# Performance work log

Measured on AMD Instinct MI355X. Metric: run time of the kernel, lower is better.

Reference implementation:

```python
import jax, jax.numpy as jnp
import numpy as np

N_EMBED = 1024
HEAD_SIZE = 128
B, T = 8, 2048

def setup_inputs() -> dict:
    key = jax.random.key(0)
    kx, kq, kk, kv = jax.random.split(key, 4)
    x = jax.random.normal(kx, (B, T, N_EMBED), dtype=jnp.float32)
    s = N_EMBED ** -0.5
    Wq = jax.random.normal(kq, (N_EMBED, HEAD_SIZE), dtype=jnp.float32) * s
    Wk = jax.random.normal(kk, (N_EMBED, HEAD_SIZE), dtype=jnp.float32) * s
    Wv = jax.random.normal(kv, (N_EMBED, HEAD_SIZE), dtype=jnp.float32) * s
    return {"x": x, "Wq": Wq, "Wk": Wk, "Wv": Wv}

def reference(x, Wq, Wk, Wv):
    # x: [B, T, C]; single causal attention head, eval mode (dropout = identity).
    Bb, Tt, C = x.shape
    q = x @ Wq  # [B, T, H]
    k = x @ Wk  # [B, T, H]
    v = x @ Wv  # [B, T, H]
    # NOTE: original scales by C**-0.5 with C = n_embed (input dim), not head_size.
    wgt = jnp.einsum('bqh,bkh->bqk', q, k) * (C ** -0.5)  # [B, T, T]
    causal = jnp.tril(jnp.ones((Tt, Tt), dtype=bool))
    wgt = jnp.where(causal, wgt, -jnp.inf)
    wgt = jax.nn.softmax(wgt, axis=-1)
    return wgt @ v  # [B, T, H]
```

## Files before the change

### kernel.cpp

```cpp
#include <hip/hip_runtime.h>
#include <hip/hip_bf16.h>

#define B_  8
#define T_  2048
#define C_  1024
#define H_  128

using f32x4  = __attribute__((ext_vector_type(4))) float;
using bf16x8 = __attribute__((ext_vector_type(8))) short;

__device__ __forceinline__ unsigned short f2bf(float f) {
    union { float f; unsigned u; } v; v.f = f;
    unsigned r = v.u + 0x7FFFu + ((v.u >> 16) & 1u);
    return (unsigned short)(r >> 16);
}

template<int C>
__device__ __forceinline__ float dppf(float v) {
    return __int_as_float(__builtin_amdgcn_update_dpp(0, __float_as_int(v), C, 0xF, 0xF, true));
}
#define DPPRED_MAX(v) { v = fmaxf(v, dppf<0xB1>(v)); v = fmaxf(v, dppf<0x4E>(v)); \
                        v = fmaxf(v, dppf<0x141>(v)); v = fmaxf(v, dppf<0x140>(v)); }
#define DPPRED_SUM(v) { v = v + dppf<0xB1>(v); v = v + dppf<0x4E>(v); \
                        v = v + dppf<0x141>(v); v = v + dppf<0x140>(v); }

__global__ void wconv_kernel(const float* __restrict__ Wq,
                             const float* __restrict__ Wk,
                             const float* __restrict__ Wv,
                             unsigned short* __restrict__ Wt) {
    int id  = blockIdx.x * 256 + threadIdx.x;
    int col = id % 384;
    int k   = id / 384;
    const float* W = (col < 128) ? Wq : ((col < 256) ? Wk : Wv);
    float v = W[k * H_ + (col & 127)];
    if (col < 128) v *= 0.03125f;
    Wt[(size_t)col * C_ + k] = f2bf(v);
}

__launch_bounds__(512, 2)
__global__ void gemm_kernel(const float* __restrict__ x,
                            const unsigned short* __restrict__ Wt,
                            unsigned short* __restrict__ qb,
                            unsigned short* __restrict__ kb,
                            unsigned short* __restrict__ vT) {
    __shared__ unsigned short As[2][64][40];

    const int tid  = threadIdx.x;
    const int wave = tid >> 6;
    const int lane = tid & 63;
    const int lo = lane & 15, hi = lane >> 4;
    const int row0 = blockIdx.x * 64;
    const int col0 = wave * 48;
    const int srow = tid >> 3;
    const int sk4  = (tid & 7) * 4;

    const float* xbase = x + (size_t)(row0 + srow) * C_ + sk4;

    f32x4 acc[4][3];
    #pragma unroll
    for (int rt = 0; rt < 4; ++rt)
        #pragma unroll
        for (int ct = 0; ct < 3; ++ct)
            acc[rt][ct] = f32x4{0.f, 0.f, 0.f, 0.f};

    float4 f0 = *(const float4*)(xbase);
    float4 f1 = *(const float4*)(xbase + 32);
    float4 f2 = *(const float4*)(xbase + 64);
    bf16x8 bc[3], bn[3];
    #pragma unroll
    for (int ct = 0; ct < 3; ++ct) {
        const unsigned short* wp = Wt + (size_t)(col0 + ct * 16 + lo) * C_ + 8 * hi;
        bc[ct] = *(const bf16x8*)(wp);
        bn[ct] = *(const bf16x8*)(wp + 32);
    }
    {
        unsigned a0 = f2bf(f0.x) | ((unsigned)f2bf(f0.y) << 16);
        unsigned a1 = f2bf(f0.z) | ((unsigned)f2bf(f0.w) << 16);
        *(uint2*)&As[0][srow][sk4] = uint2{a0, a1};
    }
    __syncthreads();

    for (int k = 0; k < 32; ++k) {
        const int cur = k & 1;

        float4 fn = f2;
        if (k < 29) fn = *(const float4*)(xbase + (k + 3) * 32);
        bf16x8 b2[3];
        const bool ldb2 = (k < 30);
        if (ldb2) {
            #pragma unroll
            for (int ct = 0; ct < 3; ++ct)
                b2[ct] = *(const bf16x8*)(Wt + (size_t)(col0 + ct * 16 + lo) * C_ + (k + 2) * 32 + 8 * hi);
        }

        bf16x8 af[4];
        #pragma unroll
        for (int rt = 0; rt < 4; ++rt)
            af[rt] = *(const bf16x8*)(&As[cur][rt * 16 + lo][8 * hi]);
        #pragma unroll
        for (int rt = 0; rt < 4; ++rt)
            #pragma unroll
            for (int ct = 0; ct < 3; ++ct)
                acc[rt][ct] = __builtin_amdgcn_mfma_f32_16x16x32_bf16(af[rt], bc[ct], acc[rt][ct], 0, 0, 0);

        if (k < 31) {
            unsigned a0 = f2bf(f1.x) | ((unsigned)f2bf(f1.y) << 16);
            unsigned a1 = f2bf(f1.z) | ((unsigned)f2bf(f1.w) << 16);
            *(uint2*)&As[cur ^ 1][srow][sk4] = uint2{a0, a1};
        }
        __syncthreads();

        f1 = f2; f2 = fn;
        bc[0] = bn[0]; bc[1] = bn[1]; bc[2] = bn[2];
        if (ldb2) { bn[0] = b2[0]; bn[1] = b2[1]; bn[2] = b2[2]; }
    }

    #pragma unroll
    for (int ct = 0; ct < 3; ++ct) {
        int col = col0 + ct * 16 + lo;
        int head = col >> 7;
        int h = col & 127;
        #pragma unroll
        for (int rt = 0; rt < 4; ++rt) {
            #pragma unroll
            for (int r = 0; r < 4; ++r) {
                int rg = row0 + rt * 16 + 4 * hi + r;
                unsigned short val = f2bf(acc[rt][ct][r]);
                if (head == 0)      qb[(size_t)rg * H_ + h] = val;
                else if (head == 1) kb[(size_t)rg * H_ + h] = val;
                else {
                    int b = rg >> 11, t = rg & (T_ - 1);
                    vT[((size_t)b * H_ + h) * T_ + t] = val;
                }
            }
        }
    }
}

__launch_bounds__(512, 2)
__global__ void attn1_kernel(const unsigned short* __restrict__ qb,
                             const unsigned short* __restrict__ kb,
                             const unsigned short* __restrict__ vT,
                             float* __restrict__ Opart,
                             float* __restrict__ MLpart) {
    __shared__ unsigned short Ks[64 * 128];
    __shared__ unsigned short Vs[128 * 64];
    __shared__ unsigned short Ps[8][16][72];

    const int tid  = threadIdx.x;
    const int wave = tid >> 6;
    const int lane = tid & 63;
    const int lo = lane & 15, hi = lane >> 4;

    const int bid   = blockIdx.x;
    const int b     = bid & 7;
    const int chunk = (bid >> 3) & 7;
    const int qt    = 7 - (bid >> 6);
    if (chunk > qt) return;

    const int kv_begin = chunk << 8;
    const size_t bT = (size_t)b * T_;
    const int qrow0 = (qt << 8) + wave * 32;

    const int krow = tid >> 3, kcol = (tid & 7) * 2;
    const int vrow = tid >> 2, vcol = (tid & 3) * 2;
    const unsigned short* kgsrc = kb + (bT + krow) * H_ + kcol * 8;
    const unsigned short* vgsrc = vT + ((size_t)b * H_ + vrow) * T_ + vcol * 8;
    unsigned short* kdst0 = &Ks[krow * 128 + ((kcol ^ (krow & 7)) * 8)];
    unsigned short* kdst1 = &Ks[krow * 128 + (((kcol + 1) ^ (krow & 7)) * 8)];
    unsigned short* vdst0 = &Vs[vrow * 64 + ((vcol ^ (vrow & 7)) * 8)];
    unsigned short* vdst1 = &Vs[vrow * 64 + (((vcol + 1) ^ (vrow & 7)) * 8)];

    bf16x8 qf[2][4];
    #pragma unroll
    for (int q2 = 0; q2 < 2; ++q2)
        #pragma unroll
        for (int kc = 0; kc < 4; ++kc)
            qf[q2][kc] = *(const bf16x8*)(qb + (bT + qrow0 + 16 * q2 + lo) * H_ + kc * 32 + 8 * hi);

    float m[2][4], l[2][4];
    f32x4 o[2][8];
    #pragma unroll
    for (int q2 = 0; q2 < 2; ++q2)
        #pragma unroll
        for (int r = 0; r < 4; ++r) { m[q2][r] = -1e30f; l[q2][r] = 0.f; }
    #pragma unroll
    for (int q2 = 0; q2 < 2; ++q2)
        #pragma unroll
        for (int ct = 0; ct < 8; ++ct) o[q2][ct] = f32x4{0.f, 0.f, 0.f, 0.f};

    uint4 kr0 = *(const uint4*)(kgsrc + (size_t)kv_begin * H_);
    uint4 kr1 = *(const uint4*)(kgsrc + (size_t)kv_begin * H_ + 8);
    uint4 vr0 = *(const uint4*)(vgsrc + kv_begin);
    uint4 vr1 = *(const uint4*)(vgsrc + kv_begin + 8);

    for (int t = 0; t < 4; ++t) {
        const int kv0 = kv_begin + t * 64;
        __syncthreads();
        *(uint4*)kdst0 = kr0;
        *(uint4*)kdst1 = kr1;
        *(uint4*)vdst0 = vr0;
        *(uint4*)vdst1 = vr1;
        __syncthreads();
        if (t < 3) {
            const int kvn = kv0 + 64;
            kr0 = *(const uint4*)(kgsrc + (size_t)kvn * H_);
            kr1 = *(const uint4*)(kgsrc + (size_t)kvn * H_ + 8);
            vr0 = *(const uint4*)(vgsrc + kvn);
            vr1 = *(const uint4*)(vgsrc + kvn + 8);
        }
        if (kv0 > qrow0 + 31) continue;

        f32x4 s[2][4];
        #pragma unroll
        for (int q2 = 0; q2 < 2; ++q2)
            #pragma unroll
            for (int ct4 = 0; ct4 < 4; ++ct4) s[q2][ct4] = f32x4{0.f, 0.f, 0.f, 0.f};
        __builtin_amdgcn_s_setprio(1);
        #pragma unroll
        for (int ct4 = 0; ct4 < 4; ++ct4) {
            const int row = ct4 * 16 + lo;
            #pragma unroll
            for (int kc = 0; kc < 4; ++kc) {
                bf16x8 kf = *(const bf16x8*)&Ks[row * 128 + (((kc * 4 + hi) ^ (row & 7)) * 8)];
                s[0][ct4] = __builtin_amdgcn_mfma_f32_16x16x32_bf16(qf[0][kc], kf, s[0][ct4], 0, 0, 0);
                s[1][ct4] = __builtin_amdgcn_mfma_f32_16x16x32_bf16(qf[1][kc], kf, s[1][ct4], 0, 0, 0);
            }
        }
        __builtin_amdgcn_s_setprio(0);

        if (kv0 + 63 >= qrow0) {
            #pragma unroll
            for (int q2 = 0; q2 < 2; ++q2)
                #pragma unroll
                for (int ct4 = 0; ct4 < 4; ++ct4)
                    #pragma unroll
                    for (int r = 0; r < 4; ++r)
                        if (kv0 + ct4 * 16 + lo > qrow0 + 16 * q2 + 4 * hi + r)
                            s[q2][ct4][r] = -1e30f;
        }

        float alpha[2][4];
        #pragma unroll
        for (int q2 = 0; q2 < 2; ++q2) {
            #pragma unroll
            for (int r = 0; r < 4; ++r) {
                float pm = fmaxf(fmaxf(s[q2][0][r], s[q2][1][r]), fmaxf(s[q2][2][r], s[q2][3][r]));
                DPPRED_MAX(pm);
                float mn = fmaxf(m[q2][r], pm);
                alpha[q2][r] = __expf(m[q2][r] - mn);
                m[q2][r] = mn;
                #pragma unroll
                for (int ct4 = 0; ct4 < 4; ++ct4) s[q2][ct4][r] = __expf(s[q2][ct4][r] - mn);
                float rs = (s[q2][0][r] + s[q2][1][r]) + (s[q2][2][r] + s[q2][3][r]);
                DPPRED_SUM(rs);
                l[q2][r] = l[q2][r] * alpha[q2][r] + rs;
            }
        }
        #pragma unroll
        for (int q2 = 0; q2 < 2; ++q2)
            #pragma unroll
            for (int ct = 0; ct < 8; ++ct)
                #pragma unroll
                for (int r = 0; r < 4; ++r) o[q2][ct][r] *= alpha[q2][r];

        bf16x8 pa[2][2];
        #pragma unroll
        for (int q2 = 0; q2 < 2; ++q2) {
            #pragma unroll
            for (int ct4 = 0; ct4 < 4; ++ct4)
                #pragma unroll
                for (int r = 0; r < 4; ++r)
                    Ps[wave][4 * hi + r][ct4 * 16 + lo] = f2bf(s[q2][ct4][r]);
            pa[q2][0] = *(const bf16x8*)&Ps[wave][lo][8 * hi];
            pa[q2][1] = *(const bf16x8*)&Ps[wave][lo][32 + 8 * hi];
        }

        __builtin_amdgcn_s_setprio(1);
        #pragma unroll
        for (int ct = 0; ct < 8; ++ct) {
            const int row = ct * 16 + lo;
            #pragma unroll
            for (int half = 0; half < 2; ++half) {
                bf16x8 vf = *(const bf16x8*)&Vs[row * 64 + (((half * 4 + hi) ^ (row & 7)) * 8)];
                o[0][ct] = __builtin_amdgcn_mfma_f32_16x16x32_bf16(pa[0][half], vf, o[0][ct], 0, 0, 0);
                o[1][ct] = __builtin_amdgcn_mfma_f32_16x16x32_bf16(pa[1][half], vf, o[1][ct], 0, 0, 0);
            }
        }
        __builtin_amdgcn_s_setprio(0);
    }

    const int slot = b * 36 + ((qt * (qt + 1)) >> 1) + chunk;
    float* op = Opart + (size_t)slot * 32768 + (size_t)(wave * 32) * 128;
    #pragma unroll
    for (int q2 = 0; q2 < 2; ++q2)
        #pragma unroll
        for (int ct = 0; ct < 8; ++ct)
            #pragma unroll
            for (int r = 0; r < 4; ++r)
                op[(16 * q2 + 4 * hi + r) * 128 + ct * 16 + lo] = o[q2][ct][r];
    if (lo == 0) {
        #pragma unroll
        for (int q2 = 0; q2 < 2; ++q2)
            #pragma unroll
            for (int r = 0; r < 4; ++r) {
                int base = slot * 512 + (wave * 32 + 16 * q2 + 4 * hi + r) * 2;
                MLpart[base]     = m[q2][r];
                MLpart[base + 1] = l[q2][r];
            }
    }
}

__launch_bounds__(128)
__global__ void attn2_kernel(const float* __restrict__ Opart,
                             const float* __restrict__ MLpart,
                             float* __restrict__ out) {
    const int bid = blockIdx.x;
    const int b   = bid & 7;
    const int qt  = (bid >> 3) & 7;
    const int sub = bid >> 6;
    const int nch = qt + 1;
    const int slot0 = b * 36 + ((qt * (qt + 1)) >> 1);

    const int tid  = threadIdx.x;
    const int row  = tid >> 2;
    const int h0   = (tid & 3) * 32;
    const int srow = sub * 32 + row;

    float M = -1e30f;
    for (int c = 0; c < nch; ++c)
        M = fmaxf(M, MLpart[(slot0 + c) * 512 + srow * 2]);
    float L = 0.f;
    for (int c = 0; c < nch; ++c) {
        float mc = MLpart[(slot0 + c) * 512 + srow * 2];
        float lc = MLpart[(slot0 + c) * 512 + srow * 2 + 1];
        L += lc * __expf(mc - M);
    }

    float4 acc[8];
    #pragma unroll
    for (int j = 0; j < 8; ++j) acc[j] = float4{0.f, 0.f, 0.f, 0.f};
    for (int c = 0; c < nch; ++c) {
        float wc = __expf(MLpart[(slot0 + c) * 512 + srow * 2] - M);
        const float4* src = (const float4*)(Opart + (size_t)(slot0 + c) * 32768 + (size_t)srow * 128 + h0);
        #pragma unroll
        for (int j = 0; j < 8; ++j) {
            float4 v = src[j];
            acc[j].x += wc * v.x; acc[j].y += wc * v.y;
            acc[j].z += wc * v.z; acc[j].w += wc * v.w;
        }
    }
    float inv = 1.f / L;
    float4* dst = (float4*)(out + ((size_t)b * T_ + qt * 256 + srow) * H_ + h0);
    #pragma unroll
    for (int j = 0; j < 8; ++j) {
        float4 v = acc[j];
        dst[j] = float4{v.x * inv, v.y * inv, v.z * inv, v.w * inv};
    }
}

extern "C" void kernel_launch(void* const* d_in, const int* in_sizes, int n_in,
                              void* d_out, int out_size, void* d_ws, size_t ws_size,
                              hipStream_t stream) {
    const float* x  = (const float*)d_in[0];
    const float* Wq = (const float*)d_in[1];
    const float* Wk = (const float*)d_in[2];
    const float* Wv = (const float*)d_in[3];
    float* out = (float*)d_out;

    char* ws = (char*)d_ws;
    unsigned short* Wt  = (unsigned short*)ws;
    unsigned short* qbf = (unsigned short*)(ws + (size_t)384 * 1024 * 2);
    unsigned short* kbf = qbf + (size_t)B_ * T_ * H_;
    unsigned short* vTf = kbf + (size_t)B_ * T_ * H_;
    float* Opart  = (float*)(vTf + (size_t)B_ * T_ * H_);
    float* MLpart = (float*)((char*)Opart + (size_t)288 * 32768 * 4);

    wconv_kernel<<<(384 * 1024) / 256, 256, 0, stream>>>(Wq, Wk, Wv, Wt);
    gemm_kernel<<<B_ * T_ / 64, 512, 0, stream>>>(x, Wt, qbf, kbf, vTf);
    attn1_kernel<<<512, 512, 0, stream>>>(qbf, kbf, vTf, Opart, MLpart);
    attn2_kernel<<<512, 128, 0, stream>>>(Opart, MLpart, out);
}
```

Before: 89.29 us.

## Retile QKV projection GEMM to 32-row blocks with 64-wide K steps

The QKV projection GEMM moves from 64-row blocks with 8 waves of 48 columns to 32-row blocks with 4 waves of 96 columns each, launching twice as many blocks. Each K step now covers 64 elements, which halves the loop trips and the number of barriers. The explicit multi-stage register prefetch of x and W fragments is dropped in favour of loading W fragments directly each iteration. This adds more blocks and fewer syncs, but re-reads W from global/L2 more often per output row and exposes W load latency without software pipelining.

```diff
diff --git a/kernel.cpp b/kernel.cpp
--- a/kernel.cpp
+++ b/kernel.cpp
@@ -37,91 +37,92 @@
     Wt[(size_t)col * C_ + k] = f2bf(v);
 }
 
-__launch_bounds__(512, 2)
+__launch_bounds__(256, 2)
 __global__ void gemm_kernel(const float* __restrict__ x,
                             const unsigned short* __restrict__ Wt,
                             unsigned short* __restrict__ qb,
                             unsigned short* __restrict__ kb,
                             unsigned short* __restrict__ vT) {
-    __shared__ unsigned short As[2][64][40];
+    __shared__ unsigned short As[2][32][72];
 
     const int tid  = threadIdx.x;
     const int wave = tid >> 6;
     const int lane = tid & 63;
     const int lo = lane & 15, hi = lane >> 4;
-    const int row0 = blockIdx.x * 64;
-    const int col0 = wave * 48;
+    const int row0 = blockIdx.x * 32;
+    const int col0 = wave * 96;
     const int srow = tid >> 3;
-    const int sk4  = (tid & 7) * 4;
-
-    const float* xbase = x + (size_t)(row0 + srow) * C_ + sk4;
-
-    f32x4 acc[4][3];
-    #pragma unroll
-    for (int rt = 0; rt < 4; ++rt)
-        #pragma unroll
-        for (int ct = 0; ct < 3; ++ct)
+    const int sk   = (tid & 7) * 8;
+
+    const float* xbase = x + (size_t)(row0 + srow) * C_ + sk;
+
+    f32x4 acc[2][6];
+    #pragma unroll
+    for (int rt = 0; rt < 2; ++rt)
+        #pragma unroll
+        for (int ct = 0; ct < 6; ++ct)
             acc[rt][ct] = f32x4{0.f, 0.f, 0.f, 0.f};
 
-    float4 f0 = *(const float4*)(xbase);
-    float4 f1 = *(const float4*)(xbase + 32);
-    float4 f2 = *(const float4*)(xbase + 64);
-    bf16x8 bc[3], bn[3];
-    #pragma unroll
-    for (int ct = 0; ct < 3; ++ct) {
-        const unsigned short* wp = Wt + (size_t)(col0 + ct * 16 + lo) * C_ + 8 * hi;
-        bc[ct] = *(const bf16x8*)(wp);
-        bn[ct] = *(const bf16x8*)(wp + 32);
-    }
     {
+        float4 f0 = *(const float4*)(xbase);
+        float4 f1 = *(const float4*)(xbase + 4);
         unsigned a0 = f2bf(f0.x) | ((unsigned)f2bf(f0.y) << 16);
         unsigned a1 = f2bf(f0.z) | ((unsigned)f2bf(f0.w) << 16);
-        *(uint2*)&As[0][srow][sk4] = uint2{a0, a1};
+        unsigned a2 = f2bf(f1.x) | ((unsigned)f2bf(f1.y) << 16);
+        unsigned a3 = f2bf(f1.z) | ((unsigned)f2bf(f1.w) << 16);
+        *(uint4*)&As[0][srow][sk] = uint4{a0, a1, a2, a3};
     }
     __syncthreads();
 
-    for (int k = 0; k < 32; ++k) {
+    for (int k = 0; k < 16; ++k) {
         const int cur = k & 1;
 
-        float4 fn = f2;
-        if (k < 29) fn = *(const float4*)(xbase + (k + 3) * 32);
-        bf16x8 b2[3];
-        const bool ldb2 = (k < 30);
-        if (ldb2) {
-            #pragma unroll
-            for (int ct = 0; ct < 3; ++ct)
-                b2[ct] = *(const bf16x8*)(Wt + (size_t)(col0 + ct * 16 + lo) * C_ + (k + 2) * 32 + 8 * hi);
-        }
-
-        bf16x8 af[4];
-        #pragma unroll
-        for (int rt = 0; rt < 4; ++rt)
-            af[rt] = *(const bf16x8*)(&As[cur][rt * 16 + lo][8 * hi]);
-        #pragma unroll
-        for (int rt = 0; rt < 4; ++rt)
-            #pragma unroll
-            for (int ct = 0; ct < 3; ++ct)
-                acc[rt][ct] = __builtin_amdgcn_mfma_f32_16x16x32_bf16(af[rt], bc[ct], acc[rt][ct], 0, 0, 0);
-
-        if (k < 31) {
-            unsigned a0 = f2bf(f1.x) | ((unsigned)f2bf(f1.y) << 16);
-            unsigned a1 = f2bf(f1.z) | ((unsigned)f2bf(f1.w) << 16);
-            *(uint2*)&As[cur ^ 1][srow][sk4] = uint2{a0, a1};
+        float4 f0, f1;
+        if (k < 15) {
+            f0 = *(const float4*)(xbase + (k + 1) * 64);
+            f1 = *(const float4*)(xbase + (k + 1) * 64 + 4);
+        }
+
+        bf16x8 bf[6][2];
+        #pragma unroll
+        for (int ct = 0; ct < 6; ++ct) {
+            const unsigned short* wp = Wt + (size_t)(col0 + ct * 16 + lo) * C_ + k * 64 + 8 * hi;
+            bf[ct][0] = *(const bf16x8*)(wp);
+            bf[ct][1] = *(const bf16x8*)(wp + 32);
+        }
+
+        bf16x8 af[2][2];
+        #pragma unroll
+        for (int rt = 0; rt < 2; ++rt)
+            #pragma unroll
+            for (int kc = 0; kc < 2; ++kc)
+                af[rt][kc] = *(const bf16x8*)(&As[cur][rt * 16 + lo][kc * 32 + 8 * hi]);
+
+        #pragma unroll
+        for (int kc = 0; kc < 2; ++kc)
+            #pragma unroll
+            for (int ct = 0; ct < 6; ++ct)
+                #pragma unroll
+                for (int rt = 0; rt < 2; ++rt)
+                    acc[rt][ct] = __builtin_amdgcn_mfma_f32_16x16x32_bf16(af[rt][kc], bf[ct][kc], acc[rt][ct], 0, 0, 0);
+
+        if (k < 15) {
+            unsigned a0 = f2bf(f0.x) | ((unsigned)f2bf(f0.y) << 16);
+            unsigned a1 = f2bf(f0.z) | ((unsigned)f2bf(f0.w) << 16);
+            unsigned a2 = f2bf(f1.x) | ((unsigned)f2bf(f1.y) << 16);
+            unsigned a3 = f2bf(f1.z) | ((unsigned)f2bf(f1.w) << 16);
+            *(uint4*)&As[cur ^ 1][srow][sk] = uint4{a0, a1, a2, a3};
         }
         __syncthreads();
-
-        f1 = f2; f2 = fn;
-        bc[0] = bn[0]; bc[1] = bn[1]; bc[2] = bn[2];
-        if (ldb2) { bn[0] = b2[0]; bn[1] = b2[1]; bn[2] = b2[2]; }
-    }
-
-    #pragma unroll
-    for (int ct = 0; ct < 3; ++ct) {
+    }
+
+    #pragma unroll
+    for (int ct = 0; ct < 6; ++ct) {
         int col = col0 + ct * 16 + lo;
         int head = col >> 7;
         int h = col & 127;
         #pragma unroll
-        for (int rt = 0; rt < 4; ++rt) {
+        for (int rt = 0; rt < 2; ++rt) {
             #pragma unroll
             for (int r = 0; r < 4; ++r) {
                 int rg = row0 + rt * 16 + 4 * hi + r;
@@ -377,7 +378,7 @@
     float* MLpart = (float*)((char*)Opart + (size_t)288 * 32768 * 4);
 
     wconv_kernel<<<(384 * 1024) / 256, 256, 0, stream>>>(Wq, Wk, Wv, Wt);
-    gemm_kernel<<<B_ * T_ / 64, 512, 0, stream>>>(x, Wt, qbf, kbf, vTf);
+    gemm_kernel<<<B_ * T_ / 32, 256, 0, stream>>>(x, Wt, qbf, kbf, vTf);
     attn1_kernel<<<512, 512, 0, stream>>>(qbf, kbf, vTf, Opart, MLpart);
     attn2_kernel<<<512, 128, 0, stream>>>(Opart, MLpart, out);
 }
```

Result: slower. 114.5 us (+28.2%).

## Stage weight tiles into LDS via direct global-to-LDS loads and split GEMM columns

Applied to the files above, without the earlier changes.

The weight conversion now writes Wt in a k-tiled, MFMA-fragment-friendly layout, so the GEMM can copy each 32-wide k slice straight into shared memory with global_load_lds instead of having every wave load B fragments from global memory into registers. The projection GEMM is split into two column halves per 64-row block, using 256-thread blocks and twice as many blocks, and the x tile load is widened to 8 floats per thread. The MFMA section is wrapped in s_setprio. This aims to cut redundant global weight traffic and register pressure and to improve occupancy, at the cost of reading and converting each x row twice across the two column-half blocks.

```diff
diff --git a/kernel.cpp b/kernel.cpp
--- a/kernel.cpp
+++ b/kernel.cpp
@@ -14,6 +14,10 @@
     unsigned r = v.u + 0x7FFFu + ((v.u >> 16) & 1u);
     return (unsigned short)(r >> 16);
 }
+
+#define GLD16(gp, lp) \
+    __builtin_amdgcn_global_load_lds((const __attribute__((address_space(1))) void*)(gp), \
+                                     (__attribute__((address_space(3))) void*)(lp), 16, 0, 0)
 
 template<int C>
 __device__ __forceinline__ float dppf(float v) {
@@ -34,27 +38,32 @@
     const float* W = (col < 128) ? Wq : ((col < 256) ? Wk : Wv);
     float v = W[k * H_ + (col & 127)];
     if (col < 128) v *= 0.03125f;
-    Wt[(size_t)col * C_ + k] = f2bf(v);
-}
-
-__launch_bounds__(512, 2)
+    const int kt = k >> 5, sub = (k >> 3) & 3, e = k & 7;
+    const int ch = col / 192, colw = col % 192;
+    Wt[(size_t)kt * 12288 + ch * 6144 + (sub * 192 + colw) * 8 + e] = f2bf(v);
+}
+
+__launch_bounds__(256, 2)
 __global__ void gemm_kernel(const float* __restrict__ x,
                             const unsigned short* __restrict__ Wt,
                             unsigned short* __restrict__ qb,
                             unsigned short* __restrict__ kb,
                             unsigned short* __restrict__ vT) {
-    __shared__ unsigned short As[2][64][40];
+    __shared__ __align__(16) unsigned short Bs[2][6144];
+    __shared__ __align__(16) unsigned short As[2][2048];
 
     const int tid  = threadIdx.x;
     const int wave = tid >> 6;
     const int lane = tid & 63;
     const int lo = lane & 15, hi = lane >> 4;
-    const int row0 = blockIdx.x * 64;
-    const int col0 = wave * 48;
-    const int srow = tid >> 3;
-    const int sk4  = (tid & 7) * 4;
-
-    const float* xbase = x + (size_t)(row0 + srow) * C_ + sk4;
+    const int rb = blockIdx.x >> 1;
+    const int ch = blockIdx.x & 1;
+    const int row0  = rb * 64;
+    const int colw0 = wave * 48;
+
+    const int arow = tid >> 2;
+    const int aq   = tid & 3;
+    const float* xsrc = x + (size_t)(row0 + arow) * C_ + aq * 8;
 
     f32x4 acc[4][3];
     #pragma unroll
@@ -63,61 +72,65 @@
         for (int ct = 0; ct < 3; ++ct)
             acc[rt][ct] = f32x4{0.f, 0.f, 0.f, 0.f};
 
-    float4 f0 = *(const float4*)(xbase);
-    float4 f1 = *(const float4*)(xbase + 32);
-    float4 f2 = *(const float4*)(xbase + 64);
-    bf16x8 bc[3], bn[3];
-    #pragma unroll
-    for (int ct = 0; ct < 3; ++ct) {
-        const unsigned short* wp = Wt + (size_t)(col0 + ct * 16 + lo) * C_ + 8 * hi;
-        bc[ct] = *(const bf16x8*)(wp);
-        bn[ct] = *(const bf16x8*)(wp + 32);
-    }
     {
-        unsigned a0 = f2bf(f0.x) | ((unsigned)f2bf(f0.y) << 16);
-        unsigned a1 = f2bf(f0.z) | ((unsigned)f2bf(f0.w) << 16);
-        *(uint2*)&As[0][srow][sk4] = uint2{a0, a1};
+        const unsigned short* g = Wt + (size_t)ch * 6144 + wave * 1536 + lane * 8;
+        #pragma unroll
+        for (int j = 0; j < 3; ++j)
+            GLD16(g + j * 512, &Bs[0][wave * 1536 + j * 512]);
+        float4 g0 = *(const float4*)(xsrc);
+        float4 g1 = *(const float4*)(xsrc + 4);
+        unsigned a0 = f2bf(g0.x) | ((unsigned)f2bf(g0.y) << 16);
+        unsigned a1 = f2bf(g0.z) | ((unsigned)f2bf(g0.w) << 16);
+        unsigned a2 = f2bf(g1.x) | ((unsigned)f2bf(g1.y) << 16);
+        unsigned a3 = f2bf(g1.z) | ((unsigned)f2bf(g1.w) << 16);
+        *(uint4*)&As[0][(aq * 64 + arow) * 8] = uint4{a0, a1, a2, a3};
     }
     __syncthreads();
 
     for (int k = 0; k < 32; ++k) {
         const int cur = k & 1;
-
-        float4 fn = f2;
-        if (k < 29) fn = *(const float4*)(xbase + (k + 3) * 32);
-        bf16x8 b2[3];
-        const bool ldb2 = (k < 30);
-        if (ldb2) {
-            #pragma unroll
-            for (int ct = 0; ct < 3; ++ct)
-                b2[ct] = *(const bf16x8*)(Wt + (size_t)(col0 + ct * 16 + lo) * C_ + (k + 2) * 32 + 8 * hi);
-        }
-
-        bf16x8 af[4];
+        const int nxt = cur ^ 1;
+
+        float4 g0, g1;
+        if (k < 31) {
+            const unsigned short* g = Wt + (size_t)(k + 1) * 12288 + ch * 6144
+                                        + wave * 1536 + lane * 8;
+            #pragma unroll
+            for (int j = 0; j < 3; ++j)
+                GLD16(g + j * 512, &Bs[nxt][wave * 1536 + j * 512]);
+            g0 = *(const float4*)(xsrc + (k + 1) * 32);
+            g1 = *(const float4*)(xsrc + (k + 1) * 32 + 4);
+        }
+
+        bf16x8 af[4], bfr[3];
         #pragma unroll
         for (int rt = 0; rt < 4; ++rt)
-            af[rt] = *(const bf16x8*)(&As[cur][rt * 16 + lo][8 * hi]);
-        #pragma unroll
-        for (int rt = 0; rt < 4; ++rt)
-            #pragma unroll
-            for (int ct = 0; ct < 3; ++ct)
-                acc[rt][ct] = __builtin_amdgcn_mfma_f32_16x16x32_bf16(af[rt], bc[ct], acc[rt][ct], 0, 0, 0);
+            af[rt] = *(const bf16x8*)&As[cur][(hi * 64 + rt * 16 + lo) * 8];
+        #pragma unroll
+        for (int ct = 0; ct < 3; ++ct)
+            bfr[ct] = *(const bf16x8*)&Bs[cur][(hi * 192 + colw0 + ct * 16 + lo) * 8];
+
+        __builtin_amdgcn_s_setprio(1);
+        #pragma unroll
+        for (int ct = 0; ct < 3; ++ct)
+            #pragma unroll
+            for (int rt = 0; rt < 4; ++rt)
+                acc[rt][ct] = __builtin_amdgcn_mfma_f32_16x16x32_bf16(af[rt], bfr[ct], acc[rt][ct], 0, 0, 0);
+        __builtin_amdgcn_s_setprio(0);
 
         if (k < 31) {
-            unsigned a0 = f2bf(f1.x) | ((unsigned)f2bf(f1.y) << 16);
-            unsigned a1 = f2bf(f1.z) | ((unsigned)f2bf(f1.w) << 16);
-            *(uint2*)&As[cur ^ 1][srow][sk4] = uint2{a0, a1};
+            unsigned a0 = f2bf(g0.x) | ((unsigned)f2bf(g0.y) << 16);
+            unsigned a1 = f2bf(g0.z) | ((unsigned)f2bf(g0.w) << 16);
+            unsigned a2 = f2bf(g1.x) | ((unsigned)f2bf(g1.y) << 16);
+            unsigned a3 = f2bf(g1.z) | ((unsigned)f2bf(g1.w) << 16);
+            *(uint4*)&As[nxt][(aq * 64 + arow) * 8] = uint4{a0, a1, a2, a3};
         }
         __syncthreads();
-
-        f1 = f2; f2 = fn;
-        bc[0] = bn[0]; bc[1] = bn[1]; bc[2] = bn[2];
-        if (ldb2) { bn[0] = b2[0]; bn[1] = b2[1]; bn[2] = b2[2]; }
     }
 
     #pragma unroll
     for (int ct = 0; ct < 3; ++ct) {
-        int col = col0 + ct * 16 + lo;
+        int col = ch * 192 + colw0 + ct * 16 + lo;
         int head = col >> 7;
         int h = col & 127;
         #pragma unroll
@@ -377,7 +390,7 @@
     float* MLpart = (float*)((char*)Opart + (size_t)288 * 32768 * 4);
 
     wconv_kernel<<<(384 * 1024) / 256, 256, 0, stream>>>(Wq, Wk, Wv, Wt);
-    gemm_kernel<<<B_ * T_ / 64, 512, 0, stream>>>(x, Wt, qbf, kbf, vTf);
+    gemm_kernel<<<B_ * T_ / 32, 256, 0, stream>>>(x, Wt, qbf, kbf, vTf);
     attn1_kernel<<<512, 512, 0, stream>>>(qbf, kbf, vTf, Opart, MLpart);
     attn2_kernel<<<512, 128, 0, stream>>>(Opart, MLpart, out);
 }
```

Measured after the change: 103.8 us. +16.2%, slower.
